# Performance work log

Measured on AMD Instinct MI355X. Metric: run time of the kernel, lower is better.

The kernel has to match this reference:

```python
import jax, jax.numpy as jnp
import numpy as np

N = 320          # number of valid codes in the batch
D = 128          # spatial dims; embeddings are (N, D+1) Lorentz points
MIN_DIST = 0.1
MARGIN = 0.1
WEIGHT = 0.1


def setup_inputs() -> dict:
    key = jax.random.key(0)
    k1, k2 = jax.random.split(key)
    # Valid hyperboloid points: x0 = sqrt(1 + ||x_spatial||^2)
    sp = 0.5 * jax.random.normal(k1, (N, D), dtype=jnp.float32)
    x0 = jnp.sqrt(1.0 + jnp.sum(sp * sp, axis=-1, keepdims=True))
    embeddings = jnp.concatenate([x0, sp], axis=-1)  # (N, D+1)
    # Symmetric nonnegative tree-distance matrix with zero diagonal
    td = jax.random.uniform(k2, (N, N), dtype=jnp.float32) * 8.0
    td = 0.5 * (td + td.T)
    td = td * (1.0 - jnp.eye(N, dtype=jnp.float32))
    return {"embeddings": embeddings, "tree_distances": td}


def _lorentz_pairwise(x):
    # Lorentz (hyperboloid) distance: d = arccosh(-<x,y>_L),
    # <x,y>_L = -x0*y0 + x_sp . y_sp
    t = x[:, :1]
    sp = x[:, 1:]
    inner = sp @ sp.T - t @ t.T  # (N, N) Minkowski inner product
    return jnp.arccosh(jnp.clip(-inner, 1.0 + 1e-7, None))


def reference(embeddings, tree_distances):
    emb = _lorentz_pairwise(embeddings)      # (N, N) embedding distances
    gt = tree_distances                       # (N, N) ground-truth distances
    n = gt.shape[0]
    # valid[a, j]: gt distance >= min_distance and j != a
    valid = (gt >= MIN_DIST) & (~jnp.eye(n, dtype=bool))
    # axes: (anchor a, j, k).  s > 0 iff gt[a,j] < gt[a,k]
    s = jnp.sign(gt[:, None, :] - gt[:, :, None])          # (N, N, N)
    diff = emb[:, :, None] - emb[:, None, :]                # e_j - e_k
    viol = jax.nn.relu(s * diff + MARGIN)                   # (N, N, N)
    tri = jnp.triu(jnp.ones((n, n), dtype=bool), 1)[None]   # j < k
    mask = valid[:, :, None] & valid[:, None, :] & tri & (s != 0.0)
    total = jnp.sum(jnp.where(mask, viol, 0.0))
    count = jnp.sum((viol > 0.0) & mask).astype(jnp.float32)
    return WEIGHT * jnp.where(count > 0.0, total / jnp.maximum(count, 1.0), 0.0)
```

## Files before the change

kernel.cpp:

```cpp
#include <hip/hip_runtime.h>
#include <math.h>

#define NN 320
#define DFULL 129
#define MIN_DIST_F 0.1f
#define MARGIN_F 0.1f
#define WEIGHT_F 0.1f
#define CHUNKJ 4
#define JLEN (NN / CHUNKJ)
#define NBLK (NN * CHUNKJ)

__global__ __launch_bounds__(256) void lorentz_kernel(const float* __restrict__ E,
                                                      float* __restrict__ emb) {
    __shared__ float As[16][DFULL];
    __shared__ float Bs[16][DFULL];
    const int i0 = blockIdx.y * 16;
    const int j0 = blockIdx.x * 16;
    for (int t = threadIdx.x; t < 16 * DFULL; t += 256) {
        int r = t / DFULL, c = t - r * DFULL;
        As[r][c] = E[(i0 + r) * DFULL + c];
        Bs[r][c] = E[(j0 + r) * DFULL + c];
    }
    __syncthreads();
    const int ti = threadIdx.x & 15;
    const int tj = threadIdx.x >> 4;
    float tt = As[tj][0] * Bs[ti][0];
    float ss = 0.0f;
    #pragma unroll
    for (int d = 1; d < DFULL; d++) ss = fmaf(As[tj][d], Bs[ti][d], ss);
    float x = fmaxf(tt - ss, 1.0f + 1e-7f);
    emb[(i0 + tj) * NN + (j0 + ti)] = acoshf(x);
}

__global__ __launch_bounds__(NN) void loss_kernel(const float* __restrict__ emb,
                                                  const float* __restrict__ gt,
                                                  float2* __restrict__ partial) {
    const int i  = blockIdx.x;
    const int j0 = blockIdx.y * JLEN;
    __shared__ float2 sge[NN];
    const int t = threadIdx.x;

    float e = emb[i * NN + t];
    float g = gt[i * NN + t];
    float gm = (g >= MIN_DIST_F && t != i) ? g : __builtin_nanf("");
    sge[t] = make_float2(e, gm);
    __syncthreads();

    const float ek = e, gk = gm;
    float total = 0.0f, cnt = 0.0f;
    #pragma unroll 4
    for (int j = j0; j < j0 + JLEN; ++j) {
        float2 u = sge[j];
        float d  = gk - u.y;
        float de = u.x - ek;
        float s  = (d > 0.0f) ? 1.0f : -1.0f;
        float v  = fmaf(s, de, MARGIN_F);
        bool vp  = (v > 0.0f) && (d > 0.0f || d < 0.0f);
        float f  = vp ? 1.0f : 0.0f;
        total = fmaf(f, v, total);
        cnt  += f;
    }

    for (int off = 32; off > 0; off >>= 1) {
        total += __shfl_down(total, off, 64);
        cnt   += __shfl_down(cnt,   off, 64);
    }
    __shared__ float wt[5], wc[5];
    const int lane = t & 63, wid = t >> 6;
    if (lane == 0) { wt[wid] = total; wc[wid] = cnt; }
    __syncthreads();
    if (t == 0) {
        float T = 0.0f, C = 0.0f;
        #pragma unroll
        for (int w = 0; w < 5; w++) { T += wt[w]; C += wc[w]; }
        partial[blockIdx.y * NN + i] = make_float2(T, C);
    }
}

__global__ __launch_bounds__(256) void finalize_kernel(const float2* __restrict__ partial,
                                                       float* __restrict__ out) {
    float T = 0.0f, C = 0.0f;
    for (int t = threadIdx.x; t < NBLK; t += 256) {
        float2 p = partial[t];
        T += p.x; C += p.y;
    }
    for (int off = 32; off > 0; off >>= 1) {
        T += __shfl_down(T, off, 64);
        C += __shfl_down(C, off, 64);
    }
    __shared__ float wt[4], wc[4];
    const int lane = threadIdx.x & 63, wid = threadIdx.x >> 6;
    if (lane == 0) { wt[wid] = T; wc[wid] = C; }
    __syncthreads();
    if (threadIdx.x == 0) {
        float Tt = wt[0] + wt[1] + wt[2] + wt[3];
        float Ct = wc[0] + wc[1] + wc[2] + wc[3];
        out[0] = (Ct > 0.0f) ? WEIGHT_F * Tt / Ct : 0.0f;
    }
}

extern "C" void kernel_launch(void* const* d_in, const int* in_sizes, int n_in,
                              void* d_out, int out_size, void* d_ws, size_t ws_size,
                              hipStream_t stream) {
    const float* E  = (const float*)d_in[0];
    const float* gt = (const float*)d_in[1];
    float* out = (float*)d_out;
    float2* partial = (float2*)d_ws;
    float*  emb = (float*)((char*)d_ws + 32768);

    dim3 g1(20, 20);
    lorentz_kernel<<<g1, 256, 0, stream>>>(E, emb);
    dim3 g2(NN, CHUNKJ);
    loss_kernel<<<g2, NN, 0, stream>>>(emb, gt, partial);
    finalize_kernel<<<1, 256, 0, stream>>>(partial, out);
}
```

Measured before the change: 21.56 us.

## Fuse Lorentz distance computation into loss kernel, drop emb intermediate

Each block now computes its own row of Lorentz distances, with each thread doing a dot product over a global row of E, and then runs the triplet loss over all j directly. This removes one kernel launch and the global round trip for the emb matrix. The j-chunking across 4 blocks is dropped, so there are 320 blocks of 320 threads, each looping over all 320 j. The cost is that every block recomputes dot products from uncoalesced per-thread row reads of E (stride 129 floats), which rely on the L2 cache. Each thread also runs a longer serial loop.

```diff
diff --git a/kernel.cpp b/kernel.cpp
--- a/kernel.cpp
+++ b/kernel.cpp
@@ -6,50 +6,35 @@
 #define MIN_DIST_F 0.1f
 #define MARGIN_F 0.1f
 #define WEIGHT_F 0.1f
-#define CHUNKJ 4
-#define JLEN (NN / CHUNKJ)
-#define NBLK (NN * CHUNKJ)
 
-__global__ __launch_bounds__(256) void lorentz_kernel(const float* __restrict__ E,
-                                                      float* __restrict__ emb) {
-    __shared__ float As[16][DFULL];
-    __shared__ float Bs[16][DFULL];
-    const int i0 = blockIdx.y * 16;
-    const int j0 = blockIdx.x * 16;
-    for (int t = threadIdx.x; t < 16 * DFULL; t += 256) {
-        int r = t / DFULL, c = t - r * DFULL;
-        As[r][c] = E[(i0 + r) * DFULL + c];
-        Bs[r][c] = E[(j0 + r) * DFULL + c];
-    }
+__global__ __launch_bounds__(NN) void fused_kernel(const float* __restrict__ E,
+                                                   const float* __restrict__ gt,
+                                                   float2* __restrict__ partial) {
+    const int i = blockIdx.x;
+    const int t = threadIdx.x;
+    __shared__ float  sEi[DFULL];
+    __shared__ float2 sge[NN];
+
+    if (t < DFULL) sEi[t] = E[i * DFULL + t];
     __syncthreads();
-    const int ti = threadIdx.x & 15;
-    const int tj = threadIdx.x >> 4;
-    float tt = As[tj][0] * Bs[ti][0];
+
+    const float* __restrict__ row = E + t * DFULL;
+    float tt = sEi[0] * row[0];
     float ss = 0.0f;
     #pragma unroll
-    for (int d = 1; d < DFULL; d++) ss = fmaf(As[tj][d], Bs[ti][d], ss);
+    for (int d = 1; d < DFULL; ++d) ss = fmaf(sEi[d], row[d], ss);
     float x = fmaxf(tt - ss, 1.0f + 1e-7f);
-    emb[(i0 + tj) * NN + (j0 + ti)] = acoshf(x);
-}
+    float e = acoshf(x);
 
-__global__ __launch_bounds__(NN) void loss_kernel(const float* __restrict__ emb,
-                                                  const float* __restrict__ gt,
-                                                  float2* __restrict__ partial) {
-    const int i  = blockIdx.x;
-    const int j0 = blockIdx.y * JLEN;
-    __shared__ float2 sge[NN];
-    const int t = threadIdx.x;
-
-    float e = emb[i * NN + t];
-    float g = gt[i * NN + t];
+    float g  = gt[i * NN + t];
     float gm = (g >= MIN_DIST_F && t != i) ? g : __builtin_nanf("");
     sge[t] = make_float2(e, gm);
     __syncthreads();
 
     const float ek = e, gk = gm;
     float total = 0.0f, cnt = 0.0f;
-    #pragma unroll 4
-    for (int j = j0; j < j0 + JLEN; ++j) {
+    #pragma unroll 8
+    for (int j = 0; j < NN; ++j) {
         float2 u = sge[j];
         float d  = gk - u.y;
         float de = u.x - ek;
@@ -73,28 +58,27 @@
         float T = 0.0f, C = 0.0f;
         #pragma unroll
         for (int w = 0; w < 5; w++) { T += wt[w]; C += wc[w]; }
-        partial[blockIdx.y * NN + i] = make_float2(T, C);
+        partial[i] = make_float2(T, C);
     }
 }
 
-__global__ __launch_bounds__(256) void finalize_kernel(const float2* __restrict__ partial,
-                                                       float* __restrict__ out) {
-    float T = 0.0f, C = 0.0f;
-    for (int t = threadIdx.x; t < NBLK; t += 256) {
-        float2 p = partial[t];
-        T += p.x; C += p.y;
-    }
+__global__ __launch_bounds__(NN) void finalize_kernel(const float2* __restrict__ partial,
+                                                      float* __restrict__ out) {
+    const int t = threadIdx.x;
+    float2 p = partial[t];
+    float T = p.x, C = p.y;
     for (int off = 32; off > 0; off >>= 1) {
         T += __shfl_down(T, off, 64);
         C += __shfl_down(C, off, 64);
     }
-    __shared__ float wt[4], wc[4];
-    const int lane = threadIdx.x & 63, wid = threadIdx.x >> 6;
+    __shared__ float wt[5], wc[5];
+    const int lane = t & 63, wid = t >> 6;
     if (lane == 0) { wt[wid] = T; wc[wid] = C; }
     __syncthreads();
-    if (threadIdx.x == 0) {
-        float Tt = wt[0] + wt[1] + wt[2] + wt[3];
-        float Ct = wc[0] + wc[1] + wc[2] + wc[3];
+    if (t == 0) {
+        float Tt = 0.0f, Ct = 0.0f;
+        #pragma unroll
+        for (int w = 0; w < 5; w++) { Tt += wt[w]; Ct += wc[w]; }
         out[0] = (Ct > 0.0f) ? WEIGHT_F * Tt / Ct : 0.0f;
     }
 }
@@ -106,11 +90,7 @@
     const float* gt = (const float*)d_in[1];
     float* out = (float*)d_out;
     float2* partial = (float2*)d_ws;
-    float*  emb = (float*)((char*)d_ws + 32768);
 
-    dim3 g1(20, 20);
-    lorentz_kernel<<<g1, 256, 0, stream>>>(E, emb);
-    dim3 g2(NN, CHUNKJ);
-    loss_kernel<<<g2, NN, 0, stream>>>(emb, gt, partial);
-    finalize_kernel<<<1, 256, 0, stream>>>(partial, out);
+    fused_kernel<<<NN, NN, 0, stream>>>(E, gt, partial);
+    finalize_kernel<<<1, NN, 0, stream>>>(partial, out);
 }
```

New measurement: 31.45 us. 1.46x slower.
